# Optimization experiments

Hardware: AMD Instinct MI355X
Metric: run time of the kernel (lower is better)

Reference implementation:

```python
import jax, jax.numpy as jnp
import numpy as np

EMBED_DIM = 512
NUM_HEADS = 8
HEAD_DIM = EMBED_DIM // NUM_HEADS  # 64
KERNEL = 3  # spatial neighborhood kernel (time kernel is full t)
EPS = 1e-6


def _rms_norm(u, gamma):
    # RMSNorm over the last (head_dim) axis
    return u * jax.lax.rsqrt(jnp.mean(u * u, axis=-1, keepdims=True) + EPS) * gamma


def _apply_rotary(x, freqs):
    # x: (b, t, h, w, nh, hd); freqs: (t, h, w, hd//2) angles
    cos = jnp.cos(freqs)[None, :, :, :, None, :]
    sin = jnp.sin(freqs)[None, :, :, :, None, :]
    xe, xo = x[..., 0::2], x[..., 1::2]
    out = jnp.stack([xe * cos - xo * sin, xe * sin + xo * cos], axis=-1)
    return out.reshape(x.shape)


def setup_inputs() -> dict:
    key = jax.random.key(0)
    ks = jax.random.split(key, 6)
    b, t, h, w = 2, 8, 32, 32
    x = jax.random.normal(ks[0], (b, t, h, w, EMBED_DIM), dtype=jnp.float32)
    freqs = jax.random.normal(ks[1], (t, h, w, HEAD_DIM // 2), dtype=jnp.float32)
    w_in = jax.random.normal(ks[2], (3 * EMBED_DIM, EMBED_DIM), dtype=jnp.float32) * 0.02
    w_out = jax.random.normal(ks[3], (EMBED_DIM, EMBED_DIM), dtype=jnp.float32) * 0.02
    q_gamma = jnp.ones((HEAD_DIM,), dtype=jnp.float32)
    k_gamma = jnp.ones((HEAD_DIM,), dtype=jnp.float32)
    return {"x": x, "freqs": freqs, "w_in": w_in, "w_out": w_out,
            "q_gamma": q_gamma, "k_gamma": k_gamma}


def reference(x, freqs, w_in, w_out, q_gamma, k_gamma):
    b, t, H, W, c = x.shape
    nh, hd = NUM_HEADS, HEAD_DIM
    # fused QKV projection (torch Linear: y = x @ W^T)
    qkv = jnp.einsum('bthwc,oc->bthwo', x, w_in).reshape(b, t, H, W, nh, 3 * hd)
    q, k, v = jnp.split(qkv, 3, axis=-1)
    q = _apply_rotary(_rms_norm(q, q_gamma), freqs)
    k = _apply_rotary(_rms_norm(k, k_gamma), freqs)
    # NATTEN 3D neighborhood: full attention over time, 3x3 spatial window
    # clamped to stay inside the feature map (window shifts near borders).
    Kc = KERNEL // 2
    ih = jnp.clip(jnp.arange(H) - Kc, 0, H - KERNEL)[:, None] + jnp.arange(KERNEL)  # (H,3)
    iw = jnp.clip(jnp.arange(W) - Kc, 0, W - KERNEL)[:, None] + jnp.arange(KERNEL)  # (W,3)

    def window(u):
        # u: (b, t, H, W, nh, hd) -> (b, H, W, nh, t*K*K, hd)
        uw = jnp.take(jnp.take(u, ih, axis=2), iw, axis=4)  # (b,t,H,K,W,K,nh,hd)
        uw = jnp.transpose(uw, (0, 2, 4, 6, 1, 3, 5, 7))     # (b,H,W,nh,t,K,K,hd)
        return uw.reshape(b, H, W, nh, t * KERNEL * KERNEL, hd)

    k_win = window(k)
    v_win = window(v)
    scale = hd ** -0.5
    scores = jnp.einsum('bthwnd,bhwnkd->bhwntk', q, k_win) * scale
    attn = jax.nn.softmax(scores, axis=-1)
    out = jnp.einsum('bhwntk,bhwnkd->bthwnd', attn, v_win)
    out = out.reshape(b, t, H, W, nh * hd)
    return jnp.einsum('bthwc,oc->bthwo', out, w_out)
```

## Files before the change

### kernel.cpp

```cpp
#include <hip/hip_runtime.h>
#include <hip/hip_bf16.h>
#include <math.h>

#define NH 8
#define C_ 512
#define C3 1536
#define NTOK 16384

typedef __attribute__((ext_vector_type(8))) short short8;
typedef __attribute__((ext_vector_type(4))) float f32x4;
typedef __attribute__((address_space(3))) void* lds_ptr_t;
typedef const __attribute__((address_space(1))) void* gbl_ptr_t;

static __device__ __forceinline__ ushort f2bf(float f) {
  __hip_bfloat16 h = __float2bfloat16(f);
  return *reinterpret_cast<ushort*>(&h);
}
static __device__ __forceinline__ float bf2f(ushort u) {
  uint t = ((uint)u) << 16;
  float f;
  __builtin_memcpy(&f, &t, 4);
  return f;
}

__global__ __launch_bounds__(256) void cast3_kernel(
    const float* __restrict__ x, const float* __restrict__ wi,
    const float* __restrict__ wo, const float* __restrict__ fr,
    ushort* __restrict__ xb, ushort* __restrict__ wib,
    ushort* __restrict__ wob, float2* __restrict__ csn) {
  const int blk = blockIdx.x;
  if (blk >= 4608) {
    int i = (blk - 4608) * 256 + threadIdx.x;
    const float4* fp = (const float4*)fr + (size_t)i * 2;
    float4 a = fp[0], b = fp[1];
    float v[8] = {a.x, a.y, a.z, a.w, b.x, b.y, b.z, b.w};
    float2 o[8];
#pragma unroll
    for (int j = 0; j < 8; ++j) { o[j].x = cosf(v[j]); o[j].y = sinf(v[j]); }
    float4* op = (float4*)(csn + (size_t)i * 8);
    op[0] = make_float4(o[0].x, o[0].y, o[1].x, o[1].y);
    op[1] = make_float4(o[2].x, o[2].y, o[3].x, o[3].y);
    op[2] = make_float4(o[4].x, o[4].y, o[5].x, o[5].y);
    op[3] = make_float4(o[6].x, o[6].y, o[7].x, o[7].y);
    return;
  }
  const float* src;
  ushort* dst;
  int i;
  if (blk < 4096)      { src = x;  dst = xb;  i = blk * 256 + threadIdx.x; }
  else if (blk < 4480) { src = wi; dst = wib; i = (blk - 4096) * 256 + threadIdx.x; }
  else                 { src = wo; dst = wob; i = (blk - 4480) * 256 + threadIdx.x; }
  const float4* p = (const float4*)src + (size_t)i * 2;
  float4 v0 = p[0], v1 = p[1];
  union { ushort u[8]; uint4 v; } r;
  r.u[0] = f2bf(v0.x); r.u[1] = f2bf(v0.y); r.u[2] = f2bf(v0.z); r.u[3] = f2bf(v0.w);
  r.u[4] = f2bf(v1.x); r.u[5] = f2bf(v1.y); r.u[6] = f2bf(v1.z); r.u[7] = f2bf(v1.w);
  *(uint4*)(dst + (size_t)i * 8) = r.v;
}

#define TBM 128
#define TBN 128
#define TBK 32
#define TILE_U ((TBM + TBN) * TBK)

static __device__ __forceinline__ void stage_tile(
    const ushort* __restrict__ A, const ushort* __restrict__ B,
    ushort* As, ushort* Bs, int bm, int bn, int K, int k0, int tid) {
#pragma unroll
  for (int it = 0; it < 2; ++it) {
    int c = it * 256 + tid;
    int row = c >> 2;
    int sk = ((c & 3) ^ ((row >> 1) & 3)) * 8;
    __builtin_amdgcn_global_load_lds(
        (gbl_ptr_t)(const void*)(A + (size_t)(bm + row) * K + k0 + sk),
        (lds_ptr_t)(As + (size_t)c * 8), 16, 0, 0);
    __builtin_amdgcn_global_load_lds(
        (gbl_ptr_t)(const void*)(B + (size_t)(bn + row) * K + k0 + sk),
        (lds_ptr_t)(Bs + (size_t)c * 8), 16, 0, 0);
  }
}

template <bool BF16OUT>
__global__ __launch_bounds__(256) void gemm_bt_bf16(
    const ushort* __restrict__ A, const ushort* __restrict__ B,
    void* __restrict__ Cv, int N, int K, int GX) {
  __shared__ ushort smem[3 * TILE_U];
  const int tid  = threadIdx.x;
  const int wave = tid >> 6;
  const int lane = tid & 63;
  const int nwg = gridDim.x;
  const int wg = (blockIdx.x & 7) * (nwg >> 3) + (blockIdx.x >> 3);
  const int bm = (wg / GX) * TBM;
  const int bn = (wg % GX) * TBN;
  const int wr = (wave >> 1) * 64;
  const int wc = (wave & 1) * 64;
  const int lm = lane & 15;
  const int g4 = lane >> 4;

  f32x4 acc[4][4];
#pragma unroll
  for (int m = 0; m < 4; ++m)
#pragma unroll
    for (int n = 0; n < 4; ++n) acc[m][n] = (f32x4){0.f, 0.f, 0.f, 0.f};

  const int ko = (g4 ^ ((lm >> 1) & 3)) * 8;

  const int nt = K / TBK;
  stage_tile(A, B, smem, smem + TBM * TBK, bm, bn, K, 0, tid);
  {
    ushort* b1 = smem + TILE_U;
    stage_tile(A, B, b1, b1 + TBM * TBK, bm, bn, K, TBK, tid);
  }
  asm volatile("s_waitcnt vmcnt(4)" ::: "memory");
  __builtin_amdgcn_s_barrier();
  asm volatile("" ::: "memory");

  for (int t = 0; t < nt; ++t) {
    if (t + 2 < nt) {
      ushort* bn3 = smem + ((t + 2) % 3) * TILE_U;
      stage_tile(A, B, bn3, bn3 + TBM * TBK, bm, bn, K, (t + 2) * TBK, tid);
    }
    const ushort* As = smem + (t % 3) * TILE_U;
    const ushort* Bs = As + TBM * TBK;
    short8 av[4], bv[4];
#pragma unroll
    for (int m = 0; m < 4; ++m)
      av[m] = *(const short8*)&As[(wr + m * 16 + lm) * TBK + ko];
#pragma unroll
    for (int n = 0; n < 4; ++n)
      bv[n] = *(const short8*)&Bs[(wc + n * 16 + lm) * TBK + ko];
#pragma unroll
    for (int m = 0; m < 4; ++m)
#pragma unroll
      for (int n = 0; n < 4; ++n)
        acc[m][n] = __builtin_amdgcn_mfma_f32_16x16x32_bf16(av[m], bv[n], acc[m][n], 0, 0, 0);
    if (t + 1 < nt) {
      if (t + 2 < nt) asm volatile("s_waitcnt vmcnt(4)" ::: "memory");
      else            asm volatile("s_waitcnt vmcnt(0)" ::: "memory");
      __builtin_amdgcn_s_barrier();
      asm volatile("" ::: "memory");
    }
  }
  __syncthreads();

  const int cr = g4 * 4;
  const int cc = lm;

  if (BF16OUT) {
    ushort* Cs = smem;
    ushort* C = (ushort*)Cv;
#pragma unroll
    for (int h = 0; h < 2; ++h) {
      __syncthreads();
      if ((wave >> 1) == h) {
#pragma unroll
        for (int m = 0; m < 4; ++m)
#pragma unroll
          for (int n = 0; n < 4; ++n)
#pragma unroll
            for (int r = 0; r < 4; ++r)
              Cs[(m * 16 + cr + r) * 128 + wc + n * 16 + cc] = f2bf(acc[m][n][r]);
      }
      __syncthreads();
#pragma unroll
      for (int i = 0; i < 4; ++i) {
        int idx = i * 256 + tid;
        int row = idx >> 4, ch = idx & 15;
        uint4 v = *(const uint4*)&Cs[row * 128 + ch * 8];
        *(uint4*)(C + (size_t)(bm + h * 64 + row) * N + bn + ch * 8) = v;
      }
    }
  } else {
    float* Csf = (float*)smem;
    float* C = (float*)Cv;
#pragma unroll
    for (int s = 0; s < 4; ++s) {
      __syncthreads();
      if ((wave >> 1) == (s >> 1)) {
#pragma unroll
        for (int mi = 0; mi < 2; ++mi)
#pragma unroll
          for (int n = 0; n < 4; ++n)
#pragma unroll
            for (int r = 0; r < 4; ++r) {
              int m = (s & 1) * 2 + mi;
              Csf[(mi * 16 + cr + r) * 128 + wc + n * 16 + cc] = acc[m][n][r];
            }
      }
      __syncthreads();
#pragma unroll
      for (int i = 0; i < 4; ++i) {
        int idx = i * 256 + tid;
        int row = idx >> 5, ch = idx & 31;
        float4 v = *(const float4*)&Csf[row * 128 + ch * 4];
        *(float4*)(C + (size_t)(bm + s * 32 + row) * N + bn + ch * 4) = v;
      }
    }
  }
}

__global__ __launch_bounds__(256) void attn_kernel(
    const ushort* __restrict__ qkv, ushort* __restrict__ outb,
    const float* __restrict__ csn, const float* __restrict__ qg,
    const float* __restrict__ kg) {
  __shared__ ushort lds[24576];
  ushort* K_s  = lds;
  ushort* Vt_s = lds + 12288;
  ushort* P_s  = lds;
  ushort* O_s  = lds + 12288;

  const int tid = threadIdx.x;
  const int wave = tid >> 6;
  const int lane = tid & 63;
  const int lin = blockIdx.x;
  const int bid = (lin & 7) * 256 + (lin >> 3);
  const int tw = bid & 7, th = (bid >> 3) & 15, n = (bid >> 7) & 7, b = bid >> 10;
  const int hb = th * 2, wb = tw * 4;
  const int hb0 = max(hb - 1, 0), wb0 = max(wb - 1, 0);
  const int lm = lane & 15, g4 = lane >> 4;

  float4 vreg[6], kreg[6];
  int mi6[6];
#pragma unroll
  for (int it = 0; it < 6; ++it) {
    int c = it * 256 + tid;
    int kr = c >> 3, gv = c & 7;
    int sc = kr >> 3, t = kr & 7;
    int kh = sc / 6, kw = sc - kh * 6;
    int hh = min(hb0 + kh, 31), ww = min(wb0 + kw, 31);
    size_t m = (((size_t)(b * 8 + t) * 32 + hh) * 32 + ww);
    mi6[it] = (int)(m & 8191);
    const ushort* bp = qkv + m * C3 + n * 192;
    vreg[it] = *(const float4*)(bp + 128 + gv * 8);
    kreg[it] = *(const float4*)(bp + 64 + gv * 8);
  }

  short8 bq[2];
  {
    int q = wave * 16 + lm;
    int tq = q >> 3, p = q & 7;
    size_t mq = (((size_t)(b * 8 + tq) * 32 + (hb + (p >> 2))) * 32 + (wb + (p & 3)));
    const ushort* qp = qkv + mq * C3 + n * 192;
    union { short8 s; ushort u[8]; } Lq0, Lq1;
    Lq0.s = *(const short8*)(qp + g4 * 8);
    Lq1.s = *(const short8*)(qp + (4 + g4) * 8);
    float fq[16];
    float ssq = 0.f;
#pragma unroll
    for (int j = 0; j < 8; ++j) { fq[j] = bf2f(Lq0.u[j]); ssq += fq[j] * fq[j]; }
#pragma unroll
    for (int j = 0; j < 8; ++j) { fq[8 + j] = bf2f(Lq1.u[j]); ssq += fq[8 + j] * fq[8 + j]; }
    ssq += __shfl_xor(ssq, 16);
    ssq += __shfl_xor(ssq, 32);
    const float rq = rsqrtf(ssq * (1.f / 64.f) + 1e-6f);
    const int miq = (int)(mq & 8191);
#pragma unroll
    for (int kk = 0; kk < 2; ++kk) {
      const int ch0 = (kk * 4 + g4) * 8;
      const float4 ga = *(const float4*)(qg + ch0);
      const float4 gb = *(const float4*)(qg + ch0 + 4);
      const float* cbp = csn + (size_t)miq * 64 + ch0;
      const float4 c0 = *(const float4*)cbp;
      const float4 c1 = *(const float4*)(cbp + 4);
      const float* fv = &fq[kk * 8];
      union { short8 s; ushort u[8]; } O;
      float xe, xo;
      xe = fv[0] * rq * ga.x; xo = fv[1] * rq * ga.y;
      O.u[0] = f2bf(xe * c0.x - xo * c0.y); O.u[1] = f2bf(xe * c0.y + xo * c0.x);
      xe = fv[2] * rq * ga.z; xo = fv[3] * rq * ga.w;
      O.u[2] = f2bf(xe * c0.z - xo * c0.w); O.u[3] = f2bf(xe * c0.w + xo * c0.z);
      xe = fv[4] * rq * gb.x; xo = fv[5] * rq * gb.y;
      O.u[4] = f2bf(xe * c1.x - xo * c1.y); O.u[5] = f2bf(xe * c1.y + xo * c1.x);
      xe = fv[6] * rq * gb.z; xo = fv[7] * rq * gb.w;
      O.u[6] = f2bf(xe * c1.z - xo * c1.w); O.u[7] = f2bf(xe * c1.w + xo * c1.z);
      bq[kk] = O.s;
    }
  }

#pragma unroll
  for (int it = 0; it < 6; ++it) {
    int c = it * 256 + tid;
    int kr = c >> 3, g = c & 7;
    union { float4 f; ushort u[8]; } L;
    L.f = kreg[it];
    float f0 = bf2f(L.u[0]), f1 = bf2f(L.u[1]), f2 = bf2f(L.u[2]), f3 = bf2f(L.u[3]);
    float f4 = bf2f(L.u[4]), f5 = bf2f(L.u[5]), f6 = bf2f(L.u[6]), f7 = bf2f(L.u[7]);
    float ss = f0 * f0 + f1 * f1 + f2 * f2 + f3 * f3 +
               f4 * f4 + f5 * f5 + f6 * f6 + f7 * f7;
    ss += __shfl_xor(ss, 1);
    ss += __shfl_xor(ss, 2);
    ss += __shfl_xor(ss, 4);
    const float rn = rsqrtf(ss * (1.f / 64.f) + 1e-6f);
    const float4 ga = *(const float4*)(kg + g * 8);
    const float4 gb = *(const float4*)(kg + g * 8 + 4);
    const float* cbp = csn + (size_t)mi6[it] * 64 + g * 8;
    const float4 c0 = *(const float4*)cbp;
    const float4 c1 = *(const float4*)(cbp + 4);
    union { short8 s; ushort u[8]; } O;
    float xe, xo;
    xe = f0 * rn * ga.x; xo = f1 * rn * ga.y;
    O.u[0] = f2bf(xe * c0.x - xo * c0.y); O.u[1] = f2bf(xe * c0.y + xo * c0.x);
    xe = f2 * rn * ga.z; xo = f3 * rn * ga.w;
    O.u[2] = f2bf(xe * c0.z - xo * c0.w); O.u[3] = f2bf(xe * c0.w + xo * c0.z);
    xe = f4 * rn * gb.x; xo = f5 * rn * gb.y;
    O.u[4] = f2bf(xe * c1.x - xo * c1.y); O.u[5] = f2bf(xe * c1.y + xo * c1.x);
    xe = f6 * rn * gb.z; xo = f7 * rn * gb.w;
    O.u[6] = f2bf(xe * c1.z - xo * c1.w); O.u[7] = f2bf(xe * c1.w + xo * c1.z);
    *(short8*)&K_s[kr * 64 + ((g ^ (kr & 7)) * 8)] = O.s;
  }

  __syncthreads();

#pragma unroll
  for (int it = 0; it < 6; ++it) {
    int c = it * 256 + tid;
    int kr = c >> 3, gv = c & 7;
    int ck = kr >> 3, kin = kr & 7;
    union { float4 f; ushort u[8]; } vv;
    vv.f = vreg[it];
#pragma unroll
    for (int j = 0; j < 8; ++j) {
      int d = gv * 8 + j;
      int cks = ck ^ ((j ^ gv) & 7);
      Vt_s[d * 192 + cks * 8 + kin] = vv.u[j];
    }
  }

  f32x4 st[12];
#pragma unroll
  for (int kf = 0; kf < 12; ++kf) st[kf] = (f32x4){0.f, 0.f, 0.f, 0.f};
#pragma unroll
  for (int kk = 0; kk < 2; ++kk)
#pragma unroll
    for (int kf = 0; kf < 12; ++kf) {
      int kr = kf * 16 + lm;
      short8 a = *(const short8*)&K_s[kr * 64 + (((kk * 4 + g4) ^ (kr & 7)) * 8)];
      st[kf] = __builtin_amdgcn_mfma_f32_16x16x32_bf16(a, bq[kk], st[kf], 0, 0, 0);
    }

  const int p = lm & 7;
  const int qh = hb + (p >> 2), qw = wb + (p & 3);
  const int loh = min(max(qh - 1, 0), 29), low = min(max(qw - 1, 0), 29);
  uint mk = 0;
#pragma unroll
  for (int kf = 0; kf < 12; ++kf) {
    int sc = kf * 2 + (g4 >> 1);
    int kh = sc / 6, kw = sc - kh * 6;
    int khg = hb0 + kh, kwg = wb0 + kw;
    bool ok = (khg >= loh) && (khg <= loh + 2) && (kwg >= low) && (kwg <= low + 2);
    mk |= (uint)ok << kf;
  }
  const float scale = 0.125f;
#pragma unroll
  for (int kf = 0; kf < 12; ++kf) {
    bool ok = (mk >> kf) & 1;
#pragma unroll
    for (int r = 0; r < 4; ++r)
      st[kf][r] = ok ? st[kf][r] * scale : -1e30f;
  }
  float mx = -1e30f;
#pragma unroll
  for (int kf = 0; kf < 12; ++kf)
#pragma unroll
    for (int r = 0; r < 4; ++r) mx = fmaxf(mx, st[kf][r]);
  mx = fmaxf(mx, __shfl_xor(mx, 16));
  mx = fmaxf(mx, __shfl_xor(mx, 32));
  float s = 0.f;
#pragma unroll
  for (int kf = 0; kf < 12; ++kf)
#pragma unroll
    for (int r = 0; r < 4; ++r) {
      float e = __expf(st[kf][r] - mx);
      st[kf][r] = e;
      s += e;
    }
  s += __shfl_xor(s, 16);
  s += __shfl_xor(s, 32);
  const float inv = 1.f / s;
  __syncthreads();

  {
    const int q = wave * 16 + lm;
    ushort* Prow = P_s + q * 192 + (g4 & 1) * 4;
#pragma unroll
    for (int kf = 0; kf < 12; ++kf) {
      uint lo = (uint)f2bf(st[kf][0] * inv) | ((uint)f2bf(st[kf][1] * inv) << 16);
      uint hi = (uint)f2bf(st[kf][2] * inv) | ((uint)f2bf(st[kf][3] * inv) << 16);
      int ck = kf * 2 + (g4 >> 1);
      int cks = ck ^ (lm & 7);
      uint2 val; val.x = lo; val.y = hi;
      *(uint2*)(Prow + cks * 8) = val;
    }
  }
  __syncthreads();

  f32x4 ao0 = (f32x4){0.f, 0.f, 0.f, 0.f};
  f32x4 ao1 = (f32x4){0.f, 0.f, 0.f, 0.f};
  f32x4 ao2 = (f32x4){0.f, 0.f, 0.f, 0.f};
  f32x4 ao3 = (f32x4){0.f, 0.f, 0.f, 0.f};
  const int drow = wave * 16 + lm;
  const int dsw = (lm & 7) ^ ((wave * 2 + (lm >> 3)) & 7);
#pragma unroll
  for (int kk = 0; kk < 6; ++kk) {
    int ch = kk * 4 + g4;
    short8 bv = *(const short8*)&Vt_s[drow * 192 + ((ch ^ dsw) * 8)];
    int pch = (ch ^ (lm & 7)) * 8;
    short8 av0 = *(const short8*)&P_s[(0 * 16 + lm) * 192 + pch];
    short8 av1 = *(const short8*)&P_s[(1 * 16 + lm) * 192 + pch];
    short8 av2 = *(const short8*)&P_s[(2 * 16 + lm) * 192 + pch];
    short8 av3 = *(const short8*)&P_s[(3 * 16 + lm) * 192 + pch];
    ao0 = __builtin_amdgcn_mfma_f32_16x16x32_bf16(av0, bv, ao0, 0, 0, 0);
    ao1 = __builtin_amdgcn_mfma_f32_16x16x32_bf16(av1, bv, ao1, 0, 0, 0);
    ao2 = __builtin_amdgcn_mfma_f32_16x16x32_bf16(av2, bv, ao2, 0, 0, 0);
    ao3 = __builtin_amdgcn_mfma_f32_16x16x32_bf16(av3, bv, ao3, 0, 0, 0);
  }
  __syncthreads();

#pragma unroll
  for (int r = 0; r < 4; ++r) {
    O_s[(0 * 16 + g4 * 4 + r) * 68 + (wave * 16 + lm)] = f2bf(ao0[r]);
    O_s[(1 * 16 + g4 * 4 + r) * 68 + (wave * 16 + lm)] = f2bf(ao1[r]);
    O_s[(2 * 16 + g4 * 4 + r) * 68 + (wave * 16 + lm)] = f2bf(ao2[r]);
    O_s[(3 * 16 + g4 * 4 + r) * 68 + (wave * 16 + lm)] = f2bf(ao3[r]);
  }
  __syncthreads();
#pragma unroll
  for (int i = 0; i < 2; ++i) {
    int idx = i * 256 + tid;
    int q = idx >> 3, c = idx & 7;
    short8 v = *(const short8*)&O_s[q * 68 + c * 8];
    int tq = q >> 3, pp = q & 7;
    size_t m = (((size_t)(b * 8 + tq) * 32 + (hb + (pp >> 2))) * 32 + (wb + (pp & 3)));
    *(short8*)(outb + m * (size_t)C_ + n * 64 + c * 8) = v;
  }
}

extern "C" void kernel_launch(void* const* d_in, const int* in_sizes, int n_in,
                              void* d_out, int out_size, void* d_ws, size_t ws_size,
                              hipStream_t stream) {
  const float* x     = (const float*)d_in[0];
  const float* freqs = (const float*)d_in[1];
  const float* w_in  = (const float*)d_in[2];
  const float* w_out = (const float*)d_in[3];
  const float* qg    = (const float*)d_in[4];
  const float* kg    = (const float*)d_in[5];
  float* out = (float*)d_out;

  char* ws = (char*)d_ws;
  ushort* qkv   = (ushort*)ws;
  ushort* xb    = (ushort*)(ws + (size_t)NTOK * C3 * 2);
  ushort* wib   = xb + (size_t)NTOK * C_;
  ushort* wob   = wib + (size_t)C3 * C_;
  ushort* attnb = wob + (size_t)C_ * C_;
  float* csn = out;

  cast3_kernel<<<4736, 256, 0, stream>>>(x, w_in, w_out, freqs, xb, wib, wob,
                                         (float2*)csn);

  gemm_bt_bf16<true><<<1536, 256, 0, stream>>>(xb, wib, qkv, C3, C_, 12);
  attn_kernel<<<2048, 256, 0, stream>>>(qkv, attnb, csn, qg, kg);
  gemm_bt_bf16<false><<<512, 256, 0, stream>>>(attnb, wob, out, C_, C_, 4);
}
```

Measured before the change: 99.81 us.

## Use 256x128 tile GEMM with 512 threads for QKV projection

Replaces the templated 128x128 QKV GEMM with a dedicated kernel that computes 256x128 output tiles using 8 waves. Each B tile is now shared across twice as many rows, and the pipeline is double-buffered with one barrier per k-step. The output staging buffer is padded to a 136-element row stride to reduce LDS bank conflicts. In exchange the grid shrinks to 768 blocks, the pipeline is shallower than the previous three-stage one, and register and LDS use per block rise.

```diff
diff --git a/kernel.cpp b/kernel.cpp
--- a/kernel.cpp
+++ b/kernel.cpp
@@ -22,6 +22,9 @@
   __builtin_memcpy(&f, &t, 4);
   return f;
 }
+
+#define GLD16(src, dst) \
+  __builtin_amdgcn_global_load_lds((gbl_ptr_t)(const void*)(src), (lds_ptr_t)(dst), 16, 0, 0)
 
 __global__ __launch_bounds__(256) void cast3_kernel(
     const float* __restrict__ x, const float* __restrict__ wi,
@@ -58,6 +61,108 @@
   *(uint4*)(dst + (size_t)i * 8) = r.v;
 }
 
+#define QBM 256
+#define QBN 128
+#define QBK 32
+#define QTILE 12288
+
+static __device__ __forceinline__ void stage_q256(
+    const ushort* __restrict__ A, const ushort* __restrict__ B,
+    ushort* As, ushort* Bs, int bm, int bn, int K, int k0, int tid) {
+#pragma unroll
+  for (int it = 0; it < 2; ++it) {
+    int c = it * 512 + tid;
+    int row = c >> 2;
+    int sk = ((c & 3) ^ ((row >> 1) & 3)) * 8;
+    GLD16(A + (size_t)(bm + row) * K + k0 + sk, As + (size_t)c * 8);
+  }
+  {
+    int c = tid;
+    int row = c >> 2;
+    int sk = ((c & 3) ^ ((row >> 1) & 3)) * 8;
+    GLD16(B + (size_t)(bn + row) * K + k0 + sk, Bs + (size_t)c * 8);
+  }
+}
+
+__global__ __launch_bounds__(512, 6) void gemm_qkv256(
+    const ushort* __restrict__ A, const ushort* __restrict__ B,
+    ushort* __restrict__ C, int N, int K, int GX) {
+  __shared__ ushort smem[2 * QTILE];
+  const int tid  = threadIdx.x;
+  const int wave = tid >> 6;
+  const int lane = tid & 63;
+  const int nwg = gridDim.x;
+  const int wg = (blockIdx.x & 7) * (nwg >> 3) + (blockIdx.x >> 3);
+  const int bm = (wg / GX) * QBM;
+  const int bn = (wg % GX) * QBN;
+  const int wr = (wave >> 1) * 64;
+  const int wc = (wave & 1) * 64;
+  const int lm = lane & 15;
+  const int g4 = lane >> 4;
+
+  f32x4 acc[4][4];
+#pragma unroll
+  for (int m = 0; m < 4; ++m)
+#pragma unroll
+    for (int n = 0; n < 4; ++n) acc[m][n] = (f32x4){0.f, 0.f, 0.f, 0.f};
+
+  const int ko = (g4 ^ ((lm >> 1) & 3)) * 8;
+
+  const int nt = K / QBK;
+  stage_q256(A, B, smem, smem + QBM * QBK, bm, bn, K, 0, tid);
+  __syncthreads();
+
+  int cur = 0;
+  for (int t = 0; t < nt; ++t) {
+    if (t + 1 < nt) {
+      ushort* nb = smem + (cur ^ 1) * QTILE;
+      stage_q256(A, B, nb, nb + QBM * QBK, bm, bn, K, (t + 1) * QBK, tid);
+    }
+    const ushort* As = smem + cur * QTILE;
+    const ushort* Bs = As + QBM * QBK;
+    short8 av[4], bv[4];
+#pragma unroll
+    for (int m = 0; m < 4; ++m)
+      av[m] = *(const short8*)&As[(wr + m * 16 + lm) * QBK + ko];
+#pragma unroll
+    for (int n = 0; n < 4; ++n)
+      bv[n] = *(const short8*)&Bs[(wc + n * 16 + lm) * QBK + ko];
+#pragma unroll
+    for (int m = 0; m < 4; ++m)
+#pragma unroll
+      for (int n = 0; n < 4; ++n)
+        acc[m][n] = __builtin_amdgcn_mfma_f32_16x16x32_bf16(av[m], bv[n], acc[m][n], 0, 0, 0);
+    __syncthreads();
+    cur ^= 1;
+  }
+
+  ushort* Cs = smem;
+  const int cr = g4 * 4;
+  const int cc = lm;
+#pragma unroll
+  for (int h = 0; h < 2; ++h) {
+    __syncthreads();
+    if ((wave >> 2) == h) {
+      const int rb = ((wave >> 1) & 1) * 64;
+#pragma unroll
+      for (int m = 0; m < 4; ++m)
+#pragma unroll
+        for (int n = 0; n < 4; ++n)
+#pragma unroll
+          for (int r = 0; r < 4; ++r)
+            Cs[(rb + m * 16 + cr + r) * 136 + wc + n * 16 + cc] = f2bf(acc[m][n][r]);
+    }
+    __syncthreads();
+#pragma unroll
+    for (int i = 0; i < 4; ++i) {
+      int idx = i * 512 + tid;
+      int row = idx >> 4, ch = idx & 15;
+      uint4 v = *(const uint4*)&Cs[row * 136 + ch * 8];
+      *(uint4*)(C + (size_t)(bm + h * 128 + row) * N + bn + ch * 8) = v;
+    }
+  }
+}
+
 #define TBM 128
 #define TBN 128
 #define TBK 32
@@ -71,19 +176,14 @@
     int c = it * 256 + tid;
     int row = c >> 2;
     int sk = ((c & 3) ^ ((row >> 1) & 3)) * 8;
-    __builtin_amdgcn_global_load_lds(
-        (gbl_ptr_t)(const void*)(A + (size_t)(bm + row) * K + k0 + sk),
-        (lds_ptr_t)(As + (size_t)c * 8), 16, 0, 0);
-    __builtin_amdgcn_global_load_lds(
-        (gbl_ptr_t)(const void*)(B + (size_t)(bn + row) * K + k0 + sk),
-        (lds_ptr_t)(Bs + (size_t)c * 8), 16, 0, 0);
-  }
-}
-
-template <bool BF16OUT>
-__global__ __launch_bounds__(256) void gemm_bt_bf16(
+    GLD16(A + (size_t)(bm + row) * K + k0 + sk, As + (size_t)c * 8);
+    GLD16(B + (size_t)(bn + row) * K + k0 + sk, Bs + (size_t)c * 8);
+  }
+}
+
+__global__ __launch_bounds__(256) void gemm_out_f32(
     const ushort* __restrict__ A, const ushort* __restrict__ B,
-    void* __restrict__ Cv, int N, int K, int GX) {
+    float* __restrict__ C, int N, int K, int GX) {
   __shared__ ushort smem[3 * TILE_U];
   const int tid  = threadIdx.x;
   const int wave = tid >> 6;
@@ -145,56 +245,28 @@
 
   const int cr = g4 * 4;
   const int cc = lm;
-
-  if (BF16OUT) {
-    ushort* Cs = smem;
-    ushort* C = (ushort*)Cv;
-#pragma unroll
-    for (int h = 0; h < 2; ++h) {
-      __syncthreads();
-      if ((wave >> 1) == h) {
-#pragma unroll
-        for (int m = 0; m < 4; ++m)
-#pragma unroll
-          for (int n = 0; n < 4; ++n)
-#pragma unroll
-            for (int r = 0; r < 4; ++r)
-              Cs[(m * 16 + cr + r) * 128 + wc + n * 16 + cc] = f2bf(acc[m][n][r]);
-      }
-      __syncthreads();
-#pragma unroll
-      for (int i = 0; i < 4; ++i) {
-        int idx = i * 256 + tid;
-        int row = idx >> 4, ch = idx & 15;
-        uint4 v = *(const uint4*)&Cs[row * 128 + ch * 8];
-        *(uint4*)(C + (size_t)(bm + h * 64 + row) * N + bn + ch * 8) = v;
-      }
-    }
-  } else {
-    float* Csf = (float*)smem;
-    float* C = (float*)Cv;
-#pragma unroll
-    for (int s = 0; s < 4; ++s) {
-      __syncthreads();
-      if ((wave >> 1) == (s >> 1)) {
-#pragma unroll
-        for (int mi = 0; mi < 2; ++mi)
-#pragma unroll
-          for (int n = 0; n < 4; ++n)
-#pragma unroll
-            for (int r = 0; r < 4; ++r) {
-              int m = (s & 1) * 2 + mi;
-              Csf[(mi * 16 + cr + r) * 128 + wc + n * 16 + cc] = acc[m][n][r];
-            }
-      }
-      __syncthreads();
-#pragma unroll
-      for (int i = 0; i < 4; ++i) {
-        int idx = i * 256 + tid;
-        int row = idx >> 5, ch = idx & 31;
-        float4 v = *(const float4*)&Csf[row * 128 + ch * 4];
-        *(float4*)(C + (size_t)(bm + s * 32 + row) * N + bn + ch * 4) = v;
-      }
+  float* Csf = (float*)smem;
+#pragma unroll
+  for (int s = 0; s < 4; ++s) {
+    __syncthreads();
+    if ((wave >> 1) == (s >> 1)) {
+#pragma unroll
+      for (int mi = 0; mi < 2; ++mi)
+#pragma unroll
+        for (int n = 0; n < 4; ++n)
+#pragma unroll
+          for (int r = 0; r < 4; ++r) {
+            int m = (s & 1) * 2 + mi;
+            Csf[(mi * 16 + cr + r) * 128 + wc + n * 16 + cc] = acc[m][n][r];
+          }
+    }
+    __syncthreads();
+#pragma unroll
+    for (int i = 0; i < 4; ++i) {
+      int idx = i * 256 + tid;
+      int row = idx >> 5, ch = idx & 31;
+      float4 v = *(const float4*)&Csf[row * 128 + ch * 4];
+      *(float4*)(C + (size_t)(bm + s * 32 + row) * N + bn + ch * 4) = v;
     }
   }
 }
@@ -457,7 +529,7 @@
   cast3_kernel<<<4736, 256, 0, stream>>>(x, w_in, w_out, freqs, xb, wib, wob,
                                          (float2*)csn);
 
-  gemm_bt_bf16<true><<<1536, 256, 0, stream>>>(xb, wib, qkv, C3, C_, 12);
+  gemm_qkv256<<<768, 512, 0, stream>>>(xb, wib, qkv, C3, C_, 12);
   attn_kernel<<<2048, 256, 0, stream>>>(qkv, attnb, csn, qg, kg);
-  gemm_bt_bf16<false><<<512, 256, 0, stream>>>(attnb, wob, out, C_, C_, 4);
-}
+  gemm_out_f32<<<512, 256, 0, stream>>>(attnb, wob, out, C_, C_, 4);
+}
```

Measured after the change: 189.8 us. 1.9x slower.

## Precompute K RMSNorm+rotary in separate pass and load K directly to LDS

Applied to the files above, without the earlier changes.

Moves the K-side RMSNorm and rotary embedding out of the attention kernel into a new standalone kernel that rewrites K in place in the qkv buffer. Each K row was previously normalized up to ~9 times across overlapping spatial windows; now it is done once. The attention kernel then streams K straight into LDS with global_load_lds, using pre-swizzled source addresses instead of going through registers. This adds an extra kernel launch and a full read/write pass over the K section of qkv.

```diff
diff --git a/kernel.cpp b/kernel.cpp
--- a/kernel.cpp
+++ b/kernel.cpp
@@ -199,10 +199,33 @@
   }
 }
 
+__global__ __launch_bounds__(256) void norm_k_kernel(
+    ushort* __restrict__ qkv, const float2* __restrict__ csn,
+    const float* __restrict__ kg) {
+  const int task = blockIdx.x * 8 + (threadIdx.x >> 5);
+  const int dp = threadIdx.x & 31;
+  const int n = task & 7;
+  const int m = task >> 3;
+  ushort* base = qkv + (size_t)m * C3 + n * 192 + 64;
+  uint val = *(uint*)(base + 2 * dp);
+  float x0 = bf2f((ushort)(val & 0xffffu));
+  float x1 = bf2f((ushort)(val >> 16));
+  float ss = x0 * x0 + x1 * x1;
+#pragma unroll
+  for (int off = 16; off >= 1; off >>= 1) ss += __shfl_xor(ss, off, 32);
+  const float r = rsqrtf(ss * (1.f / 64.f) + 1e-6f);
+  const float xe = x0 * r * kg[2 * dp];
+  const float xo = x1 * r * kg[2 * dp + 1];
+  const int mi = m & 8191;
+  float2 cs = csn[(size_t)mi * 32 + dp];
+  ushort o0 = f2bf(xe * cs.x - xo * cs.y);
+  ushort o1 = f2bf(xe * cs.y + xo * cs.x);
+  *(uint*)(base + 2 * dp) = (uint)o0 | ((uint)o1 << 16);
+}
+
 __global__ __launch_bounds__(256) void attn_kernel(
     const ushort* __restrict__ qkv, ushort* __restrict__ outb,
-    const float* __restrict__ csn, const float* __restrict__ qg,
-    const float* __restrict__ kg) {
+    const float* __restrict__ csn, const float* __restrict__ qg) {
   __shared__ ushort lds[24576];
   ushort* K_s  = lds;
   ushort* Vt_s = lds + 12288;
@@ -219,20 +242,21 @@
   const int hb0 = max(hb - 1, 0), wb0 = max(wb - 1, 0);
   const int lm = lane & 15, g4 = lane >> 4;
 
-  float4 vreg[6], kreg[6];
-  int mi6[6];
+  float4 vreg[6];
 #pragma unroll
   for (int it = 0; it < 6; ++it) {
     int c = it * 256 + tid;
     int kr = c >> 3, gv = c & 7;
+    int g = gv ^ (kr & 7);
     int sc = kr >> 3, t = kr & 7;
     int kh = sc / 6, kw = sc - kh * 6;
     int hh = min(hb0 + kh, 31), ww = min(wb0 + kw, 31);
     size_t m = (((size_t)(b * 8 + t) * 32 + hh) * 32 + ww);
-    mi6[it] = (int)(m & 8191);
     const ushort* bp = qkv + m * C3 + n * 192;
     vreg[it] = *(const float4*)(bp + 128 + gv * 8);
-    kreg[it] = *(const float4*)(bp + 64 + gv * 8);
+    __builtin_amdgcn_global_load_lds(
+        (gbl_ptr_t)(const void*)(bp + 64 + g * 8),
+        (lds_ptr_t)(K_s + (size_t)c * 8), 16, 0, 0);
   }
 
   short8 bq[2];
@@ -277,38 +301,6 @@
     }
   }
 
-#pragma unroll
-  for (int it = 0; it < 6; ++it) {
-    int c = it * 256 + tid;
-    int kr = c >> 3, g = c & 7;
-    union { float4 f; ushort u[8]; } L;
-    L.f = kreg[it];
-    float f0 = bf2f(L.u[0]), f1 = bf2f(L.u[1]), f2 = bf2f(L.u[2]), f3 = bf2f(L.u[3]);
-    float f4 = bf2f(L.u[4]), f5 = bf2f(L.u[5]), f6 = bf2f(L.u[6]), f7 = bf2f(L.u[7]);
-    float ss = f0 * f0 + f1 * f1 + f2 * f2 + f3 * f3 +
-               f4 * f4 + f5 * f5 + f6 * f6 + f7 * f7;
-    ss += __shfl_xor(ss, 1);
-    ss += __shfl_xor(ss, 2);
-    ss += __shfl_xor(ss, 4);
-    const float rn = rsqrtf(ss * (1.f / 64.f) + 1e-6f);
-    const float4 ga = *(const float4*)(kg + g * 8);
-    const float4 gb = *(const float4*)(kg + g * 8 + 4);
-    const float* cbp = csn + (size_t)mi6[it] * 64 + g * 8;
-    const float4 c0 = *(const float4*)cbp;
-    const float4 c1 = *(const float4*)(cbp + 4);
-    union { short8 s; ushort u[8]; } O;
-    float xe, xo;
-    xe = f0 * rn * ga.x; xo = f1 * rn * ga.y;
-    O.u[0] = f2bf(xe * c0.x - xo * c0.y); O.u[1] = f2bf(xe * c0.y + xo * c0.x);
-    xe = f2 * rn * ga.z; xo = f3 * rn * ga.w;
-    O.u[2] = f2bf(xe * c0.z - xo * c0.w); O.u[3] = f2bf(xe * c0.w + xo * c0.z);
-    xe = f4 * rn * gb.x; xo = f5 * rn * gb.y;
-    O.u[4] = f2bf(xe * c1.x - xo * c1.y); O.u[5] = f2bf(xe * c1.y + xo * c1.x);
-    xe = f6 * rn * gb.z; xo = f7 * rn * gb.w;
-    O.u[6] = f2bf(xe * c1.z - xo * c1.w); O.u[7] = f2bf(xe * c1.w + xo * c1.z);
-    *(short8*)&K_s[kr * 64 + ((g ^ (kr & 7)) * 8)] = O.s;
-  }
-
   __syncthreads();
 
 #pragma unroll
@@ -458,6 +450,7 @@
                                          (float2*)csn);
 
   gemm_bt_bf16<true><<<1536, 256, 0, stream>>>(xb, wib, qkv, C3, C_, 12);
-  attn_kernel<<<2048, 256, 0, stream>>>(qkv, attnb, csn, qg, kg);
+  norm_k_kernel<<<16384, 256, 0, stream>>>(qkv, (const float2*)csn, kg);
+  attn_kernel<<<2048, 256, 0, stream>>>(qkv, attnb, csn, qg);
   gemm_bt_bf16<false><<<512, 256, 0, stream>>>(attnb, wob, out, C_, C_, 4);
 }
```

After: 100.6 us. No clear change (+0.8%).

## Split attention block into K/Q and V producer warp groups with 512 threads

Applied to the files above, without the earlier changes.

Raises the attention kernel block from 256 to 512 threads. The first four waves load and normalize Q and K and then run the score, softmax and PV MFMAs. The new four waves only load V and transpose it into LDS. This spreads global loads across more waves to improve latency hiding and cut per-thread register pressure. The extra waves sit idle during the compute phases and add barrier participants, which may reduce how many blocks fit per CU.

```diff
diff --git a/kernel.cpp b/kernel.cpp
--- a/kernel.cpp
+++ b/kernel.cpp
@@ -199,7 +199,7 @@
   }
 }
 
-__global__ __launch_bounds__(256) void attn_kernel(
+__global__ __launch_bounds__(512, 2) void attn_kernel(
     const ushort* __restrict__ qkv, ushort* __restrict__ outb,
     const float* __restrict__ csn, const float* __restrict__ qg,
     const float* __restrict__ kg) {
@@ -219,167 +219,183 @@
   const int hb0 = max(hb - 1, 0), wb0 = max(wb - 1, 0);
   const int lm = lane & 15, g4 = lane >> 4;
 
-  float4 vreg[6], kreg[6];
-  int mi6[6];
-#pragma unroll
-  for (int it = 0; it < 6; ++it) {
-    int c = it * 256 + tid;
-    int kr = c >> 3, gv = c & 7;
-    int sc = kr >> 3, t = kr & 7;
-    int kh = sc / 6, kw = sc - kh * 6;
-    int hh = min(hb0 + kh, 31), ww = min(wb0 + kw, 31);
-    size_t m = (((size_t)(b * 8 + t) * 32 + hh) * 32 + ww);
-    mi6[it] = (int)(m & 8191);
-    const ushort* bp = qkv + m * C3 + n * 192;
-    vreg[it] = *(const float4*)(bp + 128 + gv * 8);
-    kreg[it] = *(const float4*)(bp + 64 + gv * 8);
-  }
-
   short8 bq[2];
-  {
-    int q = wave * 16 + lm;
-    int tq = q >> 3, p = q & 7;
-    size_t mq = (((size_t)(b * 8 + tq) * 32 + (hb + (p >> 2))) * 32 + (wb + (p & 3)));
-    const ushort* qp = qkv + mq * C3 + n * 192;
-    union { short8 s; ushort u[8]; } Lq0, Lq1;
-    Lq0.s = *(const short8*)(qp + g4 * 8);
-    Lq1.s = *(const short8*)(qp + (4 + g4) * 8);
-    float fq[16];
-    float ssq = 0.f;
-#pragma unroll
-    for (int j = 0; j < 8; ++j) { fq[j] = bf2f(Lq0.u[j]); ssq += fq[j] * fq[j]; }
-#pragma unroll
-    for (int j = 0; j < 8; ++j) { fq[8 + j] = bf2f(Lq1.u[j]); ssq += fq[8 + j] * fq[8 + j]; }
-    ssq += __shfl_xor(ssq, 16);
-    ssq += __shfl_xor(ssq, 32);
-    const float rq = rsqrtf(ssq * (1.f / 64.f) + 1e-6f);
-    const int miq = (int)(mq & 8191);
-#pragma unroll
-    for (int kk = 0; kk < 2; ++kk) {
-      const int ch0 = (kk * 4 + g4) * 8;
-      const float4 ga = *(const float4*)(qg + ch0);
-      const float4 gb = *(const float4*)(qg + ch0 + 4);
-      const float* cbp = csn + (size_t)miq * 64 + ch0;
+
+  if (tid < 256) {
+    float4 kreg[6];
+    int mi6[6];
+#pragma unroll
+    for (int it = 0; it < 6; ++it) {
+      int c = it * 256 + tid;
+      int kr = c >> 3, gv = c & 7;
+      int sc = kr >> 3, t = kr & 7;
+      int kh = sc / 6, kw = sc - kh * 6;
+      int hh = min(hb0 + kh, 31), ww = min(wb0 + kw, 31);
+      size_t m = (((size_t)(b * 8 + t) * 32 + hh) * 32 + ww);
+      mi6[it] = (int)(m & 8191);
+      kreg[it] = *(const float4*)(qkv + m * C3 + n * 192 + 64 + gv * 8);
+    }
+
+    {
+      int q = wave * 16 + lm;
+      int tq = q >> 3, p = q & 7;
+      size_t mq = (((size_t)(b * 8 + tq) * 32 + (hb + (p >> 2))) * 32 + (wb + (p & 3)));
+      const ushort* qp = qkv + mq * C3 + n * 192;
+      union { short8 s; ushort u[8]; } Lq0, Lq1;
+      Lq0.s = *(const short8*)(qp + g4 * 8);
+      Lq1.s = *(const short8*)(qp + (4 + g4) * 8);
+      float fq[16];
+      float ssq = 0.f;
+#pragma unroll
+      for (int j = 0; j < 8; ++j) { fq[j] = bf2f(Lq0.u[j]); ssq += fq[j] * fq[j]; }
+#pragma unroll
+      for (int j = 0; j < 8; ++j) { fq[8 + j] = bf2f(Lq1.u[j]); ssq += fq[8 + j] * fq[8 + j]; }
+      ssq += __shfl_xor(ssq, 16);
+      ssq += __shfl_xor(ssq, 32);
+      const float rq = rsqrtf(ssq * (1.f / 64.f) + 1e-6f);
+      const int miq = (int)(mq & 8191);
+#pragma unroll
+      for (int kk = 0; kk < 2; ++kk) {
+        const int ch0 = (kk * 4 + g4) * 8;
+        const float4 ga = *(const float4*)(qg + ch0);
+        const float4 gb = *(const float4*)(qg + ch0 + 4);
+        const float* cbp = csn + (size_t)miq * 64 + ch0;
+        const float4 c0 = *(const float4*)cbp;
+        const float4 c1 = *(const float4*)(cbp + 4);
+        const float* fv = &fq[kk * 8];
+        union { short8 s; ushort u[8]; } O;
+        float xe, xo;
+        xe = fv[0] * rq * ga.x; xo = fv[1] * rq * ga.y;
+        O.u[0] = f2bf(xe * c0.x - xo * c0.y); O.u[1] = f2bf(xe * c0.y + xo * c0.x);
+        xe = fv[2] * rq * ga.z; xo = fv[3] * rq * ga.w;
+        O.u[2] = f2bf(xe * c0.z - xo * c0.w); O.u[3] = f2bf(xe * c0.w + xo * c0.z);
+        xe = fv[4] * rq * gb.x; xo = fv[5] * rq * gb.y;
+        O.u[4] = f2bf(xe * c1.x - xo * c1.y); O.u[5] = f2bf(xe * c1.y + xo * c1.x);
+        xe = fv[6] * rq * gb.z; xo = fv[7] * rq * gb.w;
+        O.u[6] = f2bf(xe * c1.z - xo * c1.w); O.u[7] = f2bf(xe * c1.w + xo * c1.z);
+        bq[kk] = O.s;
+      }
+    }
+
+#pragma unroll
+    for (int it = 0; it < 6; ++it) {
+      int c = it * 256 + tid;
+      int kr = c >> 3, g = c & 7;
+      union { float4 f; ushort u[8]; } L;
+      L.f = kreg[it];
+      float f0 = bf2f(L.u[0]), f1 = bf2f(L.u[1]), f2 = bf2f(L.u[2]), f3 = bf2f(L.u[3]);
+      float f4 = bf2f(L.u[4]), f5 = bf2f(L.u[5]), f6 = bf2f(L.u[6]), f7 = bf2f(L.u[7]);
+      float ss = f0 * f0 + f1 * f1 + f2 * f2 + f3 * f3 +
+                 f4 * f4 + f5 * f5 + f6 * f6 + f7 * f7;
+      ss += __shfl_xor(ss, 1);
+      ss += __shfl_xor(ss, 2);
+      ss += __shfl_xor(ss, 4);
+      const float rn = rsqrtf(ss * (1.f / 64.f) + 1e-6f);
+      const float4 ga = *(const float4*)(kg + g * 8);
+      const float4 gb = *(const float4*)(kg + g * 8 + 4);
+      const float* cbp = csn + (size_t)mi6[it] * 64 + g * 8;
       const float4 c0 = *(const float4*)cbp;
       const float4 c1 = *(const float4*)(cbp + 4);
-      const float* fv = &fq[kk * 8];
       union { short8 s; ushort u[8]; } O;
       float xe, xo;
-      xe = fv[0] * rq * ga.x; xo = fv[1] * rq * ga.y;
+      xe = f0 * rn * ga.x; xo = f1 * rn * ga.y;
       O.u[0] = f2bf(xe * c0.x - xo * c0.y); O.u[1] = f2bf(xe * c0.y + xo * c0.x);
-      xe = fv[2] * rq * ga.z; xo = fv[3] * rq * ga.w;
+      xe = f2 * rn * ga.z; xo = f3 * rn * ga.w;
       O.u[2] = f2bf(xe * c0.z - xo * c0.w); O.u[3] = f2bf(xe * c0.w + xo * c0.z);
-      xe = fv[4] * rq * gb.x; xo = fv[5] * rq * gb.y;
+      xe = f4 * rn * gb.x; xo = f5 * rn * gb.y;
       O.u[4] = f2bf(xe * c1.x - xo * c1.y); O.u[5] = f2bf(xe * c1.y + xo * c1.x);
-      xe = fv[6] * rq * gb.z; xo = fv[7] * rq * gb.w;
+      xe = f6 * rn * gb.z; xo = f7 * rn * gb.w;
       O.u[6] = f2bf(xe * c1.z - xo * c1.w); O.u[7] = f2bf(xe * c1.w + xo * c1.z);
-      bq[kk] = O.s;
-    }
-  }
-
-#pragma unroll
-  for (int it = 0; it < 6; ++it) {
-    int c = it * 256 + tid;
-    int kr = c >> 3, g = c & 7;
-    union { float4 f; ushort u[8]; } L;
-    L.f = kreg[it];
-    float f0 = bf2f(L.u[0]), f1 = bf2f(L.u[1]), f2 = bf2f(L.u[2]), f3 = bf2f(L.u[3]);
-    float f4 = bf2f(L.u[4]), f5 = bf2f(L.u[5]), f6 = bf2f(L.u[6]), f7 = bf2f(L.u[7]);
-    float ss = f0 * f0 + f1 * f1 + f2 * f2 + f3 * f3 +
-               f4 * f4 + f5 * f5 + f6 * f6 + f7 * f7;
-    ss += __shfl_xor(ss, 1);
-    ss += __shfl_xor(ss, 2);
-    ss += __shfl_xor(ss, 4);
-    const float rn = rsqrtf(ss * (1.f / 64.f) + 1e-6f);
-    const float4 ga = *(const float4*)(kg + g * 8);
-    const float4 gb = *(const float4*)(kg + g * 8 + 4);
-    const float* cbp = csn + (size_t)mi6[it] * 64 + g * 8;
-    const float4 c0 = *(const float4*)cbp;
-    const float4 c1 = *(const float4*)(cbp + 4);
-    union { short8 s; ushort u[8]; } O;
-    float xe, xo;
-    xe = f0 * rn * ga.x; xo = f1 * rn * ga.y;
-    O.u[0] = f2bf(xe * c0.x - xo * c0.y); O.u[1] = f2bf(xe * c0.y + xo * c0.x);
-    xe = f2 * rn * ga.z; xo = f3 * rn * ga.w;
-    O.u[2] = f2bf(xe * c0.z - xo * c0.w); O.u[3] = f2bf(xe * c0.w + xo * c0.z);
-    xe = f4 * rn * gb.x; xo = f5 * rn * gb.y;
-    O.u[4] = f2bf(xe * c1.x - xo * c1.y); O.u[5] = f2bf(xe * c1.y + xo * c1.x);
-    xe = f6 * rn * gb.z; xo = f7 * rn * gb.w;
-    O.u[6] = f2bf(xe * c1.z - xo * c1.w); O.u[7] = f2bf(xe * c1.w + xo * c1.z);
-    *(short8*)&K_s[kr * 64 + ((g ^ (kr & 7)) * 8)] = O.s;
-  }
-
-  __syncthreads();
-
-#pragma unroll
-  for (int it = 0; it < 6; ++it) {
-    int c = it * 256 + tid;
-    int kr = c >> 3, gv = c & 7;
-    int ck = kr >> 3, kin = kr & 7;
-    union { float4 f; ushort u[8]; } vv;
-    vv.f = vreg[it];
-#pragma unroll
-    for (int j = 0; j < 8; ++j) {
-      int d = gv * 8 + j;
-      int cks = ck ^ ((j ^ gv) & 7);
-      Vt_s[d * 192 + cks * 8 + kin] = vv.u[j];
-    }
-  }
+      *(short8*)&K_s[kr * 64 + ((g ^ (kr & 7)) * 8)] = O.s;
+    }
+  } else {
+    const int t2 = tid - 256;
+    float4 vreg[6];
+#pragma unroll
+    for (int it = 0; it < 6; ++it) {
+      int c = it * 256 + t2;
+      int kr = c >> 3, gv = c & 7;
+      int sc = kr >> 3, t = kr & 7;
+      int kh = sc / 6, kw = sc - kh * 6;
+      int hh = min(hb0 + kh, 31), ww = min(wb0 + kw, 31);
+      size_t m = (((size_t)(b * 8 + t) * 32 + hh) * 32 + ww);
+      vreg[it] = *(const float4*)(qkv + m * C3 + n * 192 + 128 + gv * 8);
+    }
+#pragma unroll
+    for (int it = 0; it < 6; ++it) {
+      int c = it * 256 + t2;
+      int kr = c >> 3, gv = c & 7;
+      int ck = kr >> 3, kin = kr & 7;
+      union { float4 f; ushort u[8]; } vv;
+      vv.f = vreg[it];
+#pragma unroll
+      for (int j = 0; j < 8; ++j) {
+        int d = gv * 8 + j;
+        int cks = ck ^ ((j ^ gv) & 7);
+        Vt_s[d * 192 + cks * 8 + kin] = vv.u[j];
+      }
+    }
+  }
+
+  __syncthreads();
 
   f32x4 st[12];
 #pragma unroll
   for (int kf = 0; kf < 12; ++kf) st[kf] = (f32x4){0.f, 0.f, 0.f, 0.f};
-#pragma unroll
-  for (int kk = 0; kk < 2; ++kk)
+  float inv = 0.f;
+  if (tid < 256) {
+#pragma unroll
+    for (int kk = 0; kk < 2; ++kk)
+#pragma unroll
+      for (int kf = 0; kf < 12; ++kf) {
+        int kr = kf * 16 + lm;
+        short8 a = *(const short8*)&K_s[kr * 64 + (((kk * 4 + g4) ^ (kr & 7)) * 8)];
+        st[kf] = __builtin_amdgcn_mfma_f32_16x16x32_bf16(a, bq[kk], st[kf], 0, 0, 0);
+      }
+
+    const int p = lm & 7;
+    const int qh = hb + (p >> 2), qw = wb + (p & 3);
+    const int loh = min(max(qh - 1, 0), 29), low = min(max(qw - 1, 0), 29);
+    uint mk = 0;
 #pragma unroll
     for (int kf = 0; kf < 12; ++kf) {
-      int kr = kf * 16 + lm;
-      short8 a = *(const short8*)&K_s[kr * 64 + (((kk * 4 + g4) ^ (kr & 7)) * 8)];
-      st[kf] = __builtin_amdgcn_mfma_f32_16x16x32_bf16(a, bq[kk], st[kf], 0, 0, 0);
-    }
-
-  const int p = lm & 7;
-  const int qh = hb + (p >> 2), qw = wb + (p & 3);
-  const int loh = min(max(qh - 1, 0), 29), low = min(max(qw - 1, 0), 29);
-  uint mk = 0;
-#pragma unroll
-  for (int kf = 0; kf < 12; ++kf) {
-    int sc = kf * 2 + (g4 >> 1);
-    int kh = sc / 6, kw = sc - kh * 6;
-    int khg = hb0 + kh, kwg = wb0 + kw;
-    bool ok = (khg >= loh) && (khg <= loh + 2) && (kwg >= low) && (kwg <= low + 2);
-    mk |= (uint)ok << kf;
-  }
-  const float scale = 0.125f;
-#pragma unroll
-  for (int kf = 0; kf < 12; ++kf) {
-    bool ok = (mk >> kf) & 1;
-#pragma unroll
-    for (int r = 0; r < 4; ++r)
-      st[kf][r] = ok ? st[kf][r] * scale : -1e30f;
-  }
-  float mx = -1e30f;
-#pragma unroll
-  for (int kf = 0; kf < 12; ++kf)
-#pragma unroll
-    for (int r = 0; r < 4; ++r) mx = fmaxf(mx, st[kf][r]);
-  mx = fmaxf(mx, __shfl_xor(mx, 16));
-  mx = fmaxf(mx, __shfl_xor(mx, 32));
-  float s = 0.f;
-#pragma unroll
-  for (int kf = 0; kf < 12; ++kf)
-#pragma unroll
-    for (int r = 0; r < 4; ++r) {
-      float e = __expf(st[kf][r] - mx);
-      st[kf][r] = e;
-      s += e;
-    }
-  s += __shfl_xor(s, 16);
-  s += __shfl_xor(s, 32);
-  const float inv = 1.f / s;
-  __syncthreads();
-
-  {
+      int sc = kf * 2 + (g4 >> 1);
+      int kh = sc / 6, kw = sc - kh * 6;
+      int khg = hb0 + kh, kwg = wb0 + kw;
+      bool ok = (khg >= loh) && (khg <= loh + 2) && (kwg >= low) && (kwg <= low + 2);
+      mk |= (uint)ok << kf;
+    }
+    const float scale = 0.125f;
+#pragma unroll
+    for (int kf = 0; kf < 12; ++kf) {
+      bool ok = (mk >> kf) & 1;
+#pragma unroll
+      for (int r = 0; r < 4; ++r)
+        st[kf][r] = ok ? st[kf][r] * scale : -1e30f;
+    }
+    float mx = -1e30f;
+#pragma unroll
+    for (int kf = 0; kf < 12; ++kf)
+#pragma unroll
+      for (int r = 0; r < 4; ++r) mx = fmaxf(mx, st[kf][r]);
+    mx = fmaxf(mx, __shfl_xor(mx, 16));
+    mx = fmaxf(mx, __shfl_xor(mx, 32));
+    float s = 0.f;
+#pragma unroll
+    for (int kf = 0; kf < 12; ++kf)
+#pragma unroll
+      for (int r = 0; r < 4; ++r) {
+        float e = __expf(st[kf][r] - mx);
+        st[kf][r] = e;
+        s += e;
+      }
+    s += __shfl_xor(s, 16);
+    s += __shfl_xor(s, 32);
+    inv = 1.f / s;
+  }
+  __syncthreads();
+
+  if (tid < 256) {
     const int q = wave * 16 + lm;
     ushort* Prow = P_s + q * 192 + (g4 & 1) * 4;
 #pragma unroll
@@ -398,35 +414,38 @@
   f32x4 ao1 = (f32x4){0.f, 0.f, 0.f, 0.f};
   f32x4 ao2 = (f32x4){0.f, 0.f, 0.f, 0.f};
   f32x4 ao3 = (f32x4){0.f, 0.f, 0.f, 0.f};
-  const int drow = wave * 16 + lm;
-  const int dsw = (lm & 7) ^ ((wave * 2 + (lm >> 3)) & 7);
-#pragma unroll
-  for (int kk = 0; kk < 6; ++kk) {
-    int ch = kk * 4 + g4;
-    short8 bv = *(const short8*)&Vt_s[drow * 192 + ((ch ^ dsw) * 8)];
-    int pch = (ch ^ (lm & 7)) * 8;
-    short8 av0 = *(const short8*)&P_s[(0 * 16 + lm) * 192 + pch];
-    short8 av1 = *(const short8*)&P_s[(1 * 16 + lm) * 192 + pch];
-    short8 av2 = *(const short8*)&P_s[(2 * 16 + lm) * 192 + pch];
-    short8 av3 = *(const short8*)&P_s[(3 * 16 + lm) * 192 + pch];
-    ao0 = __builtin_amdgcn_mfma_f32_16x16x32_bf16(av0, bv, ao0, 0, 0, 0);
-    ao1 = __builtin_amdgcn_mfma_f32_16x16x32_bf16(av1, bv, ao1, 0, 0, 0);
-    ao2 = __builtin_amdgcn_mfma_f32_16x16x32_bf16(av2, bv, ao2, 0, 0, 0);
-    ao3 = __builtin_amdgcn_mfma_f32_16x16x32_bf16(av3, bv, ao3, 0, 0, 0);
-  }
-  __syncthreads();
-
-#pragma unroll
-  for (int r = 0; r < 4; ++r) {
-    O_s[(0 * 16 + g4 * 4 + r) * 68 + (wave * 16 + lm)] = f2bf(ao0[r]);
-    O_s[(1 * 16 + g4 * 4 + r) * 68 + (wave * 16 + lm)] = f2bf(ao1[r]);
-    O_s[(2 * 16 + g4 * 4 + r) * 68 + (wave * 16 + lm)] = f2bf(ao2[r]);
-    O_s[(3 * 16 + g4 * 4 + r) * 68 + (wave * 16 + lm)] = f2bf(ao3[r]);
-  }
-  __syncthreads();
-#pragma unroll
-  for (int i = 0; i < 2; ++i) {
-    int idx = i * 256 + tid;
+  if (tid < 256) {
+    const int drow = wave * 16 + lm;
+    const int dsw = (lm & 7) ^ ((wave * 2 + (lm >> 3)) & 7);
+#pragma unroll
+    for (int kk = 0; kk < 6; ++kk) {
+      int ch = kk * 4 + g4;
+      short8 bv = *(const short8*)&Vt_s[drow * 192 + ((ch ^ dsw) * 8)];
+      int pch = (ch ^ (lm & 7)) * 8;
+      short8 av0 = *(const short8*)&P_s[(0 * 16 + lm) * 192 + pch];
+      short8 av1 = *(const short8*)&P_s[(1 * 16 + lm) * 192 + pch];
+      short8 av2 = *(const short8*)&P_s[(2 * 16 + lm) * 192 + pch];
+      short8 av3 = *(const short8*)&P_s[(3 * 16 + lm) * 192 + pch];
+      ao0 = __builtin_amdgcn_mfma_f32_16x16x32_bf16(av0, bv, ao0, 0, 0, 0);
+      ao1 = __builtin_amdgcn_mfma_f32_16x16x32_bf16(av1, bv, ao1, 0, 0, 0);
+      ao2 = __builtin_amdgcn_mfma_f32_16x16x32_bf16(av2, bv, ao2, 0, 0, 0);
+      ao3 = __builtin_amdgcn_mfma_f32_16x16x32_bf16(av3, bv, ao3, 0, 0, 0);
+    }
+  }
+  __syncthreads();
+
+  if (tid < 256) {
+#pragma unroll
+    for (int r = 0; r < 4; ++r) {
+      O_s[(0 * 16 + g4 * 4 + r) * 68 + (wave * 16 + lm)] = f2bf(ao0[r]);
+      O_s[(1 * 16 + g4 * 4 + r) * 68 + (wave * 16 + lm)] = f2bf(ao1[r]);
+      O_s[(2 * 16 + g4 * 4 + r) * 68 + (wave * 16 + lm)] = f2bf(ao2[r]);
+      O_s[(3 * 16 + g4 * 4 + r) * 68 + (wave * 16 + lm)] = f2bf(ao3[r]);
+    }
+  }
+  __syncthreads();
+  {
+    int idx = tid;
     int q = idx >> 3, c = idx & 7;
     short8 v = *(const short8*)&O_s[q * 68 + c * 8];
     int tq = q >> 3, pp = q & 7;
@@ -458,6 +477,6 @@
                                          (float2*)csn);
 
   gemm_bt_bf16<true><<<1536, 256, 0, stream>>>(xb, wib, qkv, C3, C_, 12);
-  attn_kernel<<<2048, 256, 0, stream>>>(qkv, attnb, csn, qg, kg);
+  attn_kernel<<<2048, 512, 0, stream>>>(qkv, attnb, csn, qg, kg);
   gemm_bt_bf16<false><<<512, 256, 0, stream>>>(attnb, wob, out, C_, C_, 4);
 }
```

New measurement: 116.8 us. 17.1% more time.
